# Performance work log

Measured on AMD Instinct MI355X. Metric: run time of the kernel, lower is better.

Reference implementation:

```python
import jax, jax.numpy as jnp
import numpy as np

B, T, D, H = 4, 2048, 1024, 16
HD = D // H  # head_size = 64


def setup_inputs() -> dict:
    key = jax.random.key(0)
    ks = jax.random.split(key, 6)
    s = 0.02
    x = jax.random.normal(ks[0], (B, T, D), dtype=jnp.float32)
    # per-head unfused projections, stacked over heads: [H, D, HD]
    Wq = jax.random.normal(ks[1], (H, D, HD), dtype=jnp.float32) * s
    Wk = jax.random.normal(ks[2], (H, D, HD), dtype=jnp.float32) * s
    Wv = jax.random.normal(ks[3], (H, D, HD), dtype=jnp.float32) * s
    # output projection, torch Linear layout [out, in]
    Wo = jax.random.normal(ks[4], (D, D), dtype=jnp.float32) * s
    bo = jax.random.normal(ks[5], (D,), dtype=jnp.float32) * s
    return {"x": x, "Wq": Wq, "Wk": Wk, "Wv": Wv, "Wo": Wo, "bo": bo}


def reference(x, Wq, Wk, Wv, Wo, bo):
    b, t, d = x.shape
    hd = Wq.shape[-1]
    q = jnp.einsum('btd,hdk->bhtk', x, Wq)
    k = jnp.einsum('btd,hdk->bhtk', x, Wk)
    v = jnp.einsum('btd,hdk->bhtk', x, Wv)
    scores = jnp.einsum('bhtk,bhsk->bhts', q, k) / jnp.sqrt(jnp.float32(hd))
    mask = jnp.tril(jnp.ones((t, t), dtype=bool))  # causal
    scores = jnp.where(mask, scores, jnp.float32(-jnp.inf))
    p = jax.nn.softmax(scores, axis=-1)
    o = jnp.einsum('bhts,bhsk->bhtk', p, v)
    o = o.transpose(0, 2, 1, 3).reshape(b, t, d)  # concat heads
    return o @ Wo.T + bo
```

## Files before the change

### kernel.cpp

```cpp
#include <hip/hip_runtime.h>
#include <hip/hip_bf16.h>
#include <stdint.h>

#define B_   4
#define T_   2048
#define D_   1024
#define H_   16
#define HD_  64
#define MROWS (B_*T_)
#define NQKV  3072
#define NST  (T_/64)

typedef __attribute__((ext_vector_type(8))) short  short8;
typedef __attribute__((ext_vector_type(4))) short  bf16x4;
typedef __attribute__((ext_vector_type(4))) float  floatx4;

#define QSCALE 0.1803368801111244f

__device__ inline void async_copy16(const __hip_bfloat16* g, __hip_bfloat16* l) {
  __builtin_amdgcn_global_load_lds(
      (const __attribute__((address_space(1))) void*)g,
      (__attribute__((address_space(3))) void*)l, 16, 0, 0);
}

__device__ inline floatx4 mfma16(bf16x4 a, bf16x4 b, floatx4 c) {
#if __has_builtin(__builtin_amdgcn_mfma_f32_16x16x16bf16_1k)
  return __builtin_amdgcn_mfma_f32_16x16x16bf16_1k(a, b, c, 0, 0, 0);
#elif __has_builtin(__builtin_amdgcn_mfma_f32_16x16x16_bf16)
  return __builtin_amdgcn_mfma_f32_16x16x16_bf16(a, b, c, 0, 0, 0);
#else
  short8 a8 = (short8){a[0], a[1], a[2], a[3], 0, 0, 0, 0};
  short8 b8 = (short8){b[0], b[1], b[2], b[3], 0, 0, 0, 0};
  return __builtin_amdgcn_mfma_f32_16x16x32_bf16(a8, b8, c, 0, 0, 0);
#endif
}

__global__ void prep(const float* __restrict__ x, const float* __restrict__ Wo,
                     const float* __restrict__ Wq, const float* __restrict__ Wk,
                     const float* __restrict__ Wv,
                     __hip_bfloat16* __restrict__ xb, __hip_bfloat16* __restrict__ wob,
                     __hip_bfloat16* __restrict__ wqkv) {
  __shared__ __hip_bfloat16 tile[64][65];
  const int bid = (int)blockIdx.x;
  const int t = threadIdx.x;
  if (bid < 8192) {
    int i = (bid * 256 + t) * 4;
    float4 v = *(const float4*)(x + i);
    xb[i + 0] = __float2bfloat16(v.x);
    xb[i + 1] = __float2bfloat16(v.y);
    xb[i + 2] = __float2bfloat16(v.z);
    xb[i + 3] = __float2bfloat16(v.w);
  } else if (bid < 9216) {
    int i = ((bid - 8192) * 256 + t) * 4;
    float4 v = *(const float4*)(Wo + i);
    wob[i + 0] = __float2bfloat16(v.x);
    wob[i + 1] = __float2bfloat16(v.y);
    wob[i + 2] = __float2bfloat16(v.z);
    wob[i + 3] = __float2bfloat16(v.w);
  } else {
    int idx = bid - 9216;
    const int d0 = (idx & 15) * 64;
    const int wh = idx >> 4;
    const int which = wh >> 4, h = wh & 15;
    const float* W = (which == 0) ? Wq : ((which == 1) ? Wk : Wv);
    const float* base = W + (size_t)h * D_ * HD_;
#pragma unroll
    for (int i = 0; i < 16; i++) {
      int e = i * 256 + t;
      int dr = e >> 6, hd = e & 63;
      tile[dr][hd] = __float2bfloat16(base[(size_t)(d0 + dr) * HD_ + hd]);
    }
    __syncthreads();
#pragma unroll
    for (int i = 0; i < 16; i++) {
      int e = i * 256 + t;
      int hd = e >> 6, dr = e & 63;
      wqkv[(size_t)(which * 1024 + h * 64 + hd) * D_ + d0 + dr] = tile[dr][hd];
    }
  }
}

__global__ void repack_kv(const __hip_bfloat16* __restrict__ qkv,
                          __hip_bfloat16* __restrict__ kpack, __hip_bfloat16* __restrict__ vpack) {
  __shared__ __hip_bfloat16 Ks[64][72];
  __shared__ __hip_bfloat16 Vs[64][72];
  const int tid = threadIdx.x;
  const int st = blockIdx.x, bh = blockIdx.y;
  const int b = bh >> 4, h = bh & 15;
#pragma unroll
  for (int p = 0; p < 2; p++) {
    int c = p * 256 + tid;
    int row = c >> 3, col8 = c & 7;
    const __hip_bfloat16* src = qkv + (size_t)(b * T_ + st * 64 + row) * NQKV + h * HD_ + col8 * 8;
    *(uint4*)&Ks[row][col8 * 8] = *(const uint4*)(src + 1024);
    *(uint4*)&Vs[row][col8 * 8] = *(const uint4*)(src + 2048);
  }
  __syncthreads();
  const size_t base = ((size_t)bh * NST + st) * 8 * 512;
#pragma unroll
  for (int p = 0; p < 2; p++) {
    int pair = p * 256 + tid;
    int c = pair >> 6, l = pair & 63;
    int lq = l & 15, q = l >> 4;
    int ni = c >> 1, half = c & 1;
    short8 v = *(const short8*)&Ks[ni * 16 + lq][half * 32 + q * 8];
    *(short8*)(kpack + base + (size_t)c * 512 + l * 8) = v;
  }
#pragma unroll
  for (int p = 0; p < 2; p++) {
    int pair = p * 256 + tid;
    int c = pair >> 6, l = pair & 63;
    int lq = l & 15, q = l >> 4;
    int m = c >> 2, nt = c & 3;
    __hip_bfloat16 tmp[8];
#pragma unroll
    for (int half = 0; half < 2; half++)
#pragma unroll
      for (int j = 0; j < 4; j++)
        tmp[half * 4 + j] = Vs[(2 * m + half) * 16 + q * 4 + j][nt * 16 + lq];
    *(short8*)(vpack + base + (size_t)c * 512 + l * 8) = *(short8*)tmp;
  }
}


__device__ inline void stage16k(const __hip_bfloat16* __restrict__ grow0, int K,
                                short* ldst, int tid) {
#pragma unroll
  for (int l = 0; l < 2; ++l) {
    int c = l * 512 + tid;
    int r = c >> 3;
    int sw = (c & 7) ^ (r & 7);
    async_copy16(grow0 + (size_t)r * K + sw * 8, (__hip_bfloat16*)(ldst + c * 8));
  }
}

__device__ inline short8 fragld2(const short* base, int r, int slot) {
  return *(const short8*)(base + r * 64 + (((slot) ^ (r & 7)) << 3));
}

__launch_bounds__(512, 2)
__global__ void gemmq(const __hip_bfloat16* __restrict__ A, const __hip_bfloat16* __restrict__ Bt,
                      __hip_bfloat16* __restrict__ Cb, int M, int N, int K, float qscale) {
  __shared__ short LDS[2][32768];
  const int tid = threadIdx.x;
  const int lane = tid & 63, wid = tid >> 6;
  const int lq = lane & 15, quad = lane >> 4;
  const int wr = wid >> 2, wc = wid & 3;

  const int lin = (int)blockIdx.x;
  const int s = (lin & 7) * 64 + (lin >> 3);
  const int m0 = (s & 63) * 128, n0 = (s >> 6) * 384;

  const int NT = K >> 6;

  floatx4 acc[4][6];
#pragma unroll
  for (int i = 0; i < 4; i++)
#pragma unroll
    for (int j = 0; j < 6; j++) acc[i][j] = (floatx4){0.f, 0.f, 0.f, 0.f};

  {
    short* b0 = &LDS[0][0];
    stage16k(A + (size_t)m0 * K, K, b0, tid);
#pragma unroll
    for (int j = 0; j < 3; ++j)
      stage16k(Bt + (size_t)(n0 + 128 * j) * K, K, b0 + 8192 + 8192 * j, tid);
  }

#pragma unroll 1
  for (int t = 0; t < NT; ++t) {
    __syncthreads();
    const short* buf = &LDS[t & 1][0];
    short* nb = &LDS[(t & 1) ^ 1][0];
    const int kc = (t + 1) << 6;

    short8 a0[4], b0[6];
#pragma unroll
    for (int mi = 0; mi < 4; ++mi)
      a0[mi] = fragld2(buf, wr * 64 + mi * 16 + lq, quad);
#pragma unroll
    for (int ni = 0; ni < 6; ++ni)
      b0[ni] = fragld2(buf + 8192, wc * 96 + ni * 16 + lq, quad);
    if (t + 1 < NT) {
      stage16k(A + (size_t)m0 * K + kc, K, nb, tid);
#pragma unroll
      for (int j = 0; j < 3; ++j)
        stage16k(Bt + (size_t)(n0 + 128 * j) * K + kc, K, nb + 8192 + 8192 * j, tid);
    }
    __builtin_amdgcn_s_setprio(1);
#pragma unroll
    for (int mi = 0; mi < 4; ++mi)
#pragma unroll
      for (int ni = 0; ni < 6; ++ni)
        acc[mi][ni] = __builtin_amdgcn_mfma_f32_16x16x32_bf16(a0[mi], b0[ni], acc[mi][ni], 0, 0, 0);
    __builtin_amdgcn_s_setprio(0);

    short8 a1[4], b1[6];
#pragma unroll
    for (int mi = 0; mi < 4; ++mi)
      a1[mi] = fragld2(buf, wr * 64 + mi * 16 + lq, 4 + quad);
#pragma unroll
    for (int ni = 0; ni < 6; ++ni)
      b1[ni] = fragld2(buf + 8192, wc * 96 + ni * 16 + lq, 4 + quad);
    __builtin_amdgcn_s_setprio(1);
#pragma unroll
    for (int mi = 0; mi < 4; ++mi)
#pragma unroll
      for (int ni = 0; ni < 6; ++ni)
        acc[mi][ni] = __builtin_amdgcn_mfma_f32_16x16x32_bf16(a1[mi], b1[ni], acc[mi][ni], 0, 0, 0);
    __builtin_amdgcn_s_setprio(0);
  }

#pragma unroll
  for (int mi = 0; mi < 4; ++mi) {
#pragma unroll
    for (int ni = 0; ni < 6; ++ni) {
      int col = n0 + wc * 96 + ni * 16 + lq;
      float sc = (col < 1024) ? qscale : 1.0f;
#pragma unroll
      for (int r = 0; r < 4; ++r) {
        int row = m0 + wr * 64 + mi * 16 + quad * 4 + r;
        Cb[(size_t)row * N + col] = __float2bfloat16(acc[mi][ni][r] * sc);
      }
    }
  }
}

__launch_bounds__(512, 2)
__global__ void gemmo(const __hip_bfloat16* __restrict__ A, const __hip_bfloat16* __restrict__ Bt,
                      float* __restrict__ Cf, const float* __restrict__ bias,
                      int M, int N, int K) {
  __shared__ short LDS[2][24576];
  const int tid = threadIdx.x;
  const int lane = tid & 63, wid = tid >> 6;
  const int lq = lane & 15, quad = lane >> 4;
  const int wr = wid >> 2, wc = wid & 3;

  const int lin = (int)blockIdx.x;
  const int s = (lin & 7) * 32 + (lin >> 3);
  const int m0 = (s & 63) * 128, n0 = (s >> 6) * 256;

  const int NT = K >> 6;

  floatx4 acc[4][4];
#pragma unroll
  for (int i = 0; i < 4; i++)
#pragma unroll
    for (int j = 0; j < 4; j++) acc[i][j] = (floatx4){0.f, 0.f, 0.f, 0.f};

  {
    short* b0 = &LDS[0][0];
    stage16k(A + (size_t)m0 * K, K, b0, tid);
    stage16k(Bt + (size_t)n0 * K, K, b0 + 8192, tid);
    stage16k(Bt + (size_t)(n0 + 128) * K, K, b0 + 16384, tid);
  }

#pragma unroll 1
  for (int t = 0; t < NT; ++t) {
    __syncthreads();
    const short* buf = &LDS[t & 1][0];
    short* nb = &LDS[(t & 1) ^ 1][0];
    const int kc = (t + 1) << 6;

    short8 a0[4], b0[4];
#pragma unroll
    for (int mi = 0; mi < 4; ++mi)
      a0[mi] = fragld2(buf, wr * 64 + mi * 16 + lq, quad);
#pragma unroll
    for (int ni = 0; ni < 4; ++ni)
      b0[ni] = fragld2(buf + 8192, wc * 64 + ni * 16 + lq, quad);
    if (t + 1 < NT) {
      stage16k(A + (size_t)m0 * K + kc, K, nb, tid);
      stage16k(Bt + (size_t)n0 * K + kc, K, nb + 8192, tid);
      stage16k(Bt + (size_t)(n0 + 128) * K + kc, K, nb + 16384, tid);
    }
    __builtin_amdgcn_s_setprio(1);
#pragma unroll
    for (int mi = 0; mi < 4; ++mi)
#pragma unroll
      for (int ni = 0; ni < 4; ++ni)
        acc[mi][ni] = __builtin_amdgcn_mfma_f32_16x16x32_bf16(a0[mi], b0[ni], acc[mi][ni], 0, 0, 0);
    __builtin_amdgcn_s_setprio(0);

    short8 a1[4], b1[4];
#pragma unroll
    for (int mi = 0; mi < 4; ++mi)
      a1[mi] = fragld2(buf, wr * 64 + mi * 16 + lq, 4 + quad);
#pragma unroll
    for (int ni = 0; ni < 4; ++ni)
      b1[ni] = fragld2(buf + 8192, wc * 64 + ni * 16 + lq, 4 + quad);
    __builtin_amdgcn_s_setprio(1);
#pragma unroll
    for (int mi = 0; mi < 4; ++mi)
#pragma unroll
      for (int ni = 0; ni < 4; ++ni)
        acc[mi][ni] = __builtin_amdgcn_mfma_f32_16x16x32_bf16(a1[mi], b1[ni], acc[mi][ni], 0, 0, 0);
    __builtin_amdgcn_s_setprio(0);
  }

#pragma unroll
  for (int mi = 0; mi < 4; ++mi) {
#pragma unroll
    for (int ni = 0; ni < 4; ++ni) {
      int col = n0 + wc * 64 + ni * 16 + lq;
      float bv = bias[col];
#pragma unroll
      for (int r = 0; r < 4; ++r) {
        int row = m0 + wr * 64 + mi * 16 + quad * 4 + r;
        Cf[(size_t)row * N + col] = acc[mi][ni][r] + bv;
      }
    }
  }
}

__launch_bounds__(256, 2)
__global__ void attn(const __hip_bfloat16* __restrict__ qkv,
                     const __hip_bfloat16* __restrict__ kpack,
                     const __hip_bfloat16* __restrict__ vpack,
                     __hip_bfloat16* __restrict__ obuf) {
  __shared__ __hip_bfloat16 KVs[2][8192];
  const int tid = threadIdx.x;
  const int w = tid >> 6, lane = tid & 63;
  const int lq = lane & 15, quad = lane >> 4;

  const int bh = (int)blockIdx.x;
  const int a  = (int)blockIdx.y;
  const int b = bh >> 4, h = bh & 15;

  const __hip_bfloat16* kbase = kpack + ((size_t)bh * NST) * 4096;
  const __hip_bfloat16* vbase = vpack + ((size_t)bh * NST) * 4096;

#pragma unroll 1
  for (int seg = 0; seg < 2; ++seg) {
    const int tbase = seg ? (NST - 2 - 2 * a) : (2 * a);
    const int qt = tbase + (w >> 1);
    const int rbase = (w & 1) * 32;

    short8 qf[2][2];
#pragma unroll
    for (int bi = 0; bi < 2; bi++) {
      const __hip_bfloat16* qp =
          qkv + ((size_t)(b * T_ + qt * 64 + rbase + bi * 16 + lq)) * NQKV + h * HD_;
      qf[bi][0] = *(const short8*)(qp + quad * 8);
      qf[bi][1] = *(const short8*)(qp + 32 + quad * 8);
    }

    floatx4 Oacc[2][4];
#pragma unroll
    for (int bi = 0; bi < 2; bi++)
#pragma unroll
      for (int i = 0; i < 4; i++) Oacc[bi][i] = (floatx4){0.f, 0.f, 0.f, 0.f};
    float lrow[2] = {0.f, 0.f};

    const int itTop = tbase + 1;

#pragma unroll
    for (int j = 0; j < 2; ++j) {
      int c = j * 256 + tid;
      async_copy16(kbase + (size_t)c * 8, &KVs[0][0] + c * 8);
      async_copy16(vbase + (size_t)c * 8, &KVs[0][4096] + c * 8);
    }
    __syncthreads();

#pragma unroll 1
    for (int it = 0; it <= itTop; ++it) {
      const int cur = it & 1;
      if (it < itTop) {
        const __hip_bfloat16* kn = kbase + (size_t)(it + 1) * 4096;
        const __hip_bfloat16* vn = vbase + (size_t)(it + 1) * 4096;
#pragma unroll
        for (int j = 0; j < 2; ++j) {
          int c = j * 256 + tid;
          async_copy16(kn + (size_t)c * 8, &KVs[cur ^ 1][0] + c * 8);
          async_copy16(vn + (size_t)c * 8, &KVs[cur ^ 1][4096] + c * 8);
        }
      }
      if (it <= qt) {
        const __hip_bfloat16* Kb = &KVs[cur][0] + lane * 8;
        const __hip_bfloat16* Vb = &KVs[cur][4096] + lane * 8;
        short8 kf[4], kg[4];
#pragma unroll
        for (int ni = 0; ni < 4; ni++) {
          kf[ni] = *(const short8*)(Kb + (size_t)(ni * 2 + 0) * 512);
          kg[ni] = *(const short8*)(Kb + (size_t)(ni * 2 + 1) * 512);
        }
        short8 vfr[8];
#pragma unroll
        for (int c = 0; c < 8; c++) vfr[c] = *(const short8*)(Vb + (size_t)c * 512);

        floatx4 Sc[2][4];
        __builtin_amdgcn_s_setprio(1);
#pragma unroll
        for (int bi = 0; bi < 2; bi++)
#pragma unroll
          for (int ni = 0; ni < 4; ni++) {
            floatx4 c0 = (floatx4){0.f, 0.f, 0.f, 0.f};
            c0 = __builtin_amdgcn_mfma_f32_16x16x32_bf16(kf[ni], qf[bi][0], c0, 0, 0, 0);
            c0 = __builtin_amdgcn_mfma_f32_16x16x32_bf16(kg[ni], qf[bi][1], c0, 0, 0, 0);
            Sc[bi][ni] = c0;
          }
        __builtin_amdgcn_s_setprio(0);

        if (it == qt) {
#pragma unroll
          for (int bi = 0; bi < 2; bi++) {
            int lrow_idx = rbase + bi * 16 + lq;
#pragma unroll
            for (int ni = 0; ni < 4; ni++)
#pragma unroll
              for (int r = 0; r < 4; r++) {
                int s_loc = ni * 16 + quad * 4 + r;
                if (s_loc > lrow_idx) Sc[bi][ni][r] = -__builtin_inff();
              }
          }
        }

        bf16x4 pf[2][4];
#pragma unroll
        for (int bi = 0; bi < 2; bi++)
#pragma unroll
          for (int c = 0; c < 4; c++) {
            __hip_bfloat16 pb[4];
#pragma unroll
            for (int r = 0; r < 4; r++) {
              float p = __builtin_amdgcn_exp2f(Sc[bi][c][r]);
              lrow[bi] += p;
              pb[r] = __float2bfloat16(p);
            }
            pf[bi][c] = *(bf16x4*)pb;
          }

        __builtin_amdgcn_s_setprio(1);
#pragma unroll
        for (int m = 0; m < 2; m++)
#pragma unroll
          for (int nt = 0; nt < 4; nt++) {
            short8 v8 = vfr[m * 4 + nt];
            bf16x4 vlo = (bf16x4){v8[0], v8[1], v8[2], v8[3]};
            bf16x4 vhi = (bf16x4){v8[4], v8[5], v8[6], v8[7]};
#pragma unroll
            for (int bi = 0; bi < 2; bi++) {
              Oacc[bi][nt] = mfma16(pf[bi][2 * m + 0], vlo, Oacc[bi][nt]);
              Oacc[bi][nt] = mfma16(pf[bi][2 * m + 1], vhi, Oacc[bi][nt]);
            }
          }
        __builtin_amdgcn_s_setprio(0);
      }
      __syncthreads();
    }

#pragma unroll
    for (int bi = 0; bi < 2; bi++) {
      float ps = lrow[bi];
      ps += __shfl_xor(ps, 16);
      ps += __shfl_xor(ps, 32);
      float inv = 1.0f / ps;
#pragma unroll
      for (int r = 0; r < 4; r++) {
        float invr = __shfl(inv, quad * 4 + r);
        int t = qt * 64 + rbase + bi * 16 + quad * 4 + r;
#pragma unroll
        for (int nt = 0; nt < 4; nt++)
          obuf[(size_t)(b * T_ + t) * D_ + h * HD_ + nt * 16 + lq] =
              __float2bfloat16(Oacc[bi][nt][r] * invr);
      }
    }
  }
}


extern "C" void kernel_launch(void* const* d_in, const int* in_sizes, int n_in,
                              void* d_out, int out_size, void* d_ws, size_t ws_size,
                              hipStream_t stream) {
  const float* x  = (const float*)d_in[0];
  const float* Wq = (const float*)d_in[1];
  const float* Wk = (const float*)d_in[2];
  const float* Wv = (const float*)d_in[3];
  const float* Wo = (const float*)d_in[4];
  const float* bo = (const float*)d_in[5];
  float* out = (float*)d_out;

  char* ws = (char*)d_ws;
  __hip_bfloat16* xb    = (__hip_bfloat16*)(ws);
  __hip_bfloat16* obuf  = (__hip_bfloat16*)(ws);
  __hip_bfloat16* wqkv  = (__hip_bfloat16*)(ws + ((size_t)16 << 20));
  __hip_bfloat16* wob   = (__hip_bfloat16*)(ws + ((size_t)22 << 20));
  __hip_bfloat16* qkv   = (__hip_bfloat16*)(ws + ((size_t)24 << 20));
  __hip_bfloat16* kpack = (__hip_bfloat16*)(ws + ((size_t)72 << 20));
  __hip_bfloat16* vpack = (__hip_bfloat16*)(ws + ((size_t)88 << 20));

  prep<<<9984, 256, 0, stream>>>(x, Wo, Wq, Wk, Wv, xb, wob, wqkv);

  gemmq<<<512, 512, 0, stream>>>(xb, wqkv, qkv, MROWS, NQKV, D_, QSCALE);

  repack_kv<<<dim3(NST, B_ * H_), 256, 0, stream>>>(qkv, kpack, vpack);

  attn<<<dim3(B_ * H_, 8), 256, 0, stream>>>(qkv, kpack, vpack, obuf);

  gemmo<<<256, 512, 0, stream>>>(obuf, wob, out, bo, MROWS, D_, D_);
}
```

Baseline: 247.9 us.

## Double KV tile per attention stage and retile output GEMM to 128x128

```diff
diff --git a/kernel.cpp b/kernel.cpp
--- a/kernel.cpp
+++ b/kernel.cpp
@@ -123,11 +123,12 @@
 }
 
 
+template <int THR>
 __device__ inline void stage16k(const __hip_bfloat16* __restrict__ grow0, int K,
                                 short* ldst, int tid) {
 #pragma unroll
-  for (int l = 0; l < 2; ++l) {
-    int c = l * 512 + tid;
+  for (int l = 0; l < 1024 / THR; ++l) {
+    int c = l * THR + tid;
     int r = c >> 3;
     int sw = (c & 7) ^ (r & 7);
     async_copy16(grow0 + (size_t)r * K + sw * 8, (__hip_bfloat16*)(ldst + c * 8));
@@ -161,10 +162,10 @@
 
   {
     short* b0 = &LDS[0][0];
-    stage16k(A + (size_t)m0 * K, K, b0, tid);
+    stage16k<512>(A + (size_t)m0 * K, K, b0, tid);
 #pragma unroll
     for (int j = 0; j < 3; ++j)
-      stage16k(Bt + (size_t)(n0 + 128 * j) * K, K, b0 + 8192 + 8192 * j, tid);
+      stage16k<512>(Bt + (size_t)(n0 + 128 * j) * K, K, b0 + 8192 + 8192 * j, tid);
   }
 
 #pragma unroll 1
@@ -182,10 +183,10 @@
     for (int ni = 0; ni < 6; ++ni)
       b0[ni] = fragld2(buf + 8192, wc * 96 + ni * 16 + lq, quad);
     if (t + 1 < NT) {
-      stage16k(A + (size_t)m0 * K + kc, K, nb, tid);
+      stage16k<512>(A + (size_t)m0 * K + kc, K, nb, tid);
 #pragma unroll
       for (int j = 0; j < 3; ++j)
-        stage16k(Bt + (size_t)(n0 + 128 * j) * K + kc, K, nb + 8192 + 8192 * j, tid);
+        stage16k<512>(Bt + (size_t)(n0 + 128 * j) * K + kc, K, nb + 8192 + 8192 * j, tid);
     }
     __builtin_amdgcn_s_setprio(1);
 #pragma unroll
@@ -226,19 +227,19 @@
   }
 }
 
-__launch_bounds__(512, 2)
-__global__ void gemmo(const __hip_bfloat16* __restrict__ A, const __hip_bfloat16* __restrict__ Bt,
+__launch_bounds__(256, 2)
+__global__ void gemmp(const __hip_bfloat16* __restrict__ A, const __hip_bfloat16* __restrict__ Bt,
                       float* __restrict__ Cf, const float* __restrict__ bias,
                       int M, int N, int K) {
-  __shared__ short LDS[2][24576];
+  __shared__ short LDS[2][16384];
   const int tid = threadIdx.x;
   const int lane = tid & 63, wid = tid >> 6;
   const int lq = lane & 15, quad = lane >> 4;
-  const int wr = wid >> 2, wc = wid & 3;
+  const int wr = wid >> 1, wc = wid & 1;
 
   const int lin = (int)blockIdx.x;
-  const int s = (lin & 7) * 32 + (lin >> 3);
-  const int m0 = (s & 63) * 128, n0 = (s >> 6) * 256;
+  const int s = (lin & 7) * 64 + (lin >> 3);
+  const int m0 = (s & 63) * 128, n0 = (s >> 6) * 128;
 
   const int NT = K >> 6;
 
@@ -248,12 +249,8 @@
 #pragma unroll
     for (int j = 0; j < 4; j++) acc[i][j] = (floatx4){0.f, 0.f, 0.f, 0.f};
 
-  {
-    short* b0 = &LDS[0][0];
-    stage16k(A + (size_t)m0 * K, K, b0, tid);
-    stage16k(Bt + (size_t)n0 * K, K, b0 + 8192, tid);
-    stage16k(Bt + (size_t)(n0 + 128) * K, K, b0 + 16384, tid);
-  }
+  stage16k<256>(A + (size_t)m0 * K, K, &LDS[0][0], tid);
+  stage16k<256>(Bt + (size_t)n0 * K, K, &LDS[0][8192], tid);
 
 #pragma unroll 1
   for (int t = 0; t < NT; ++t) {
@@ -270,9 +267,8 @@
     for (int ni = 0; ni < 4; ++ni)
       b0[ni] = fragld2(buf + 8192, wc * 64 + ni * 16 + lq, quad);
     if (t + 1 < NT) {
-      stage16k(A + (size_t)m0 * K + kc, K, nb, tid);
-      stage16k(Bt + (size_t)n0 * K + kc, K, nb + 8192, tid);
-      stage16k(Bt + (size_t)(n0 + 128) * K + kc, K, nb + 16384, tid);
+      stage16k<256>(A + (size_t)m0 * K + kc, K, nb, tid);
+      stage16k<256>(Bt + (size_t)n0 * K + kc, K, nb + 8192, tid);
     }
     __builtin_amdgcn_s_setprio(1);
 #pragma unroll
@@ -318,7 +314,7 @@
                      const __hip_bfloat16* __restrict__ kpack,
                      const __hip_bfloat16* __restrict__ vpack,
                      __hip_bfloat16* __restrict__ obuf) {
-  __shared__ __hip_bfloat16 KVs[2][8192];
+  __shared__ __hip_bfloat16 KVs[2][16384];
   const int tid = threadIdx.x;
   const int w = tid >> 6, lane = tid & 63;
   const int lq = lane & 15, quad = lane >> 4;
@@ -352,101 +348,108 @@
       for (int i = 0; i < 4; i++) Oacc[bi][i] = (floatx4){0.f, 0.f, 0.f, 0.f};
     float lrow[2] = {0.f, 0.f};
 
-    const int itTop = tbase + 1;
-
-#pragma unroll
-    for (int j = 0; j < 2; ++j) {
+    const int pTop = tbase >> 1;
+
+#pragma unroll
+    for (int j = 0; j < 4; ++j) {
       int c = j * 256 + tid;
       async_copy16(kbase + (size_t)c * 8, &KVs[0][0] + c * 8);
-      async_copy16(vbase + (size_t)c * 8, &KVs[0][4096] + c * 8);
-    }
-    __syncthreads();
-
+      async_copy16(vbase + (size_t)c * 8, &KVs[0][8192] + c * 8);
+    }
+    asm volatile("s_waitcnt vmcnt(0)" ::: "memory");
+    __builtin_amdgcn_s_barrier();
+
+    int cur = 0;
 #pragma unroll 1
-    for (int it = 0; it <= itTop; ++it) {
-      const int cur = it & 1;
-      if (it < itTop) {
-        const __hip_bfloat16* kn = kbase + (size_t)(it + 1) * 4096;
-        const __hip_bfloat16* vn = vbase + (size_t)(it + 1) * 4096;
-#pragma unroll
-        for (int j = 0; j < 2; ++j) {
+    for (int p = 0; p <= pTop; ++p) {
+      if (p < pTop) {
+        const __hip_bfloat16* kn = kbase + (size_t)(2 * (p + 1)) * 4096;
+        const __hip_bfloat16* vn = vbase + (size_t)(2 * (p + 1)) * 4096;
+#pragma unroll
+        for (int j = 0; j < 4; ++j) {
           int c = j * 256 + tid;
           async_copy16(kn + (size_t)c * 8, &KVs[cur ^ 1][0] + c * 8);
-          async_copy16(vn + (size_t)c * 8, &KVs[cur ^ 1][4096] + c * 8);
+          async_copy16(vn + (size_t)c * 8, &KVs[cur ^ 1][8192] + c * 8);
         }
       }
-      if (it <= qt) {
-        const __hip_bfloat16* Kb = &KVs[cur][0] + lane * 8;
-        const __hip_bfloat16* Vb = &KVs[cur][4096] + lane * 8;
-        short8 kf[4], kg[4];
-#pragma unroll
-        for (int ni = 0; ni < 4; ni++) {
-          kf[ni] = *(const short8*)(Kb + (size_t)(ni * 2 + 0) * 512);
-          kg[ni] = *(const short8*)(Kb + (size_t)(ni * 2 + 1) * 512);
-        }
-        short8 vfr[8];
-#pragma unroll
-        for (int c = 0; c < 8; c++) vfr[c] = *(const short8*)(Vb + (size_t)c * 512);
-
-        floatx4 Sc[2][4];
-        __builtin_amdgcn_s_setprio(1);
-#pragma unroll
-        for (int bi = 0; bi < 2; bi++)
+#pragma unroll
+      for (int f = 0; f < 2; ++f) {
+        const int t64 = 2 * p + f;
+        if (t64 <= qt) {
+          const __hip_bfloat16* Kb = &KVs[cur][f * 4096] + lane * 8;
+          const __hip_bfloat16* Vb = &KVs[cur][8192 + f * 4096] + lane * 8;
+          short8 kf[4], kg[4];
 #pragma unroll
           for (int ni = 0; ni < 4; ni++) {
-            floatx4 c0 = (floatx4){0.f, 0.f, 0.f, 0.f};
-            c0 = __builtin_amdgcn_mfma_f32_16x16x32_bf16(kf[ni], qf[bi][0], c0, 0, 0, 0);
-            c0 = __builtin_amdgcn_mfma_f32_16x16x32_bf16(kg[ni], qf[bi][1], c0, 0, 0, 0);
-            Sc[bi][ni] = c0;
+            kf[ni] = *(const short8*)(Kb + (size_t)(ni * 2 + 0) * 512);
+            kg[ni] = *(const short8*)(Kb + (size_t)(ni * 2 + 1) * 512);
           }
-        __builtin_amdgcn_s_setprio(0);
-
-        if (it == qt) {
-#pragma unroll
-          for (int bi = 0; bi < 2; bi++) {
-            int lrow_idx = rbase + bi * 16 + lq;
-#pragma unroll
-            for (int ni = 0; ni < 4; ni++)
-#pragma unroll
-              for (int r = 0; r < 4; r++) {
-                int s_loc = ni * 16 + quad * 4 + r;
-                if (s_loc > lrow_idx) Sc[bi][ni][r] = -__builtin_inff();
-              }
-          }
-        }
-
-        bf16x4 pf[2][4];
-#pragma unroll
-        for (int bi = 0; bi < 2; bi++)
-#pragma unroll
-          for (int c = 0; c < 4; c++) {
-            __hip_bfloat16 pb[4];
-#pragma unroll
-            for (int r = 0; r < 4; r++) {
-              float p = __builtin_amdgcn_exp2f(Sc[bi][c][r]);
-              lrow[bi] += p;
-              pb[r] = __float2bfloat16(p);
+          short8 vfr[8];
+#pragma unroll
+          for (int c = 0; c < 8; c++) vfr[c] = *(const short8*)(Vb + (size_t)c * 512);
+
+          floatx4 Sc[2][4];
+          __builtin_amdgcn_s_setprio(1);
+#pragma unroll
+          for (int bi = 0; bi < 2; bi++)
+#pragma unroll
+            for (int ni = 0; ni < 4; ni++) {
+              floatx4 c0 = (floatx4){0.f, 0.f, 0.f, 0.f};
+              c0 = __builtin_amdgcn_mfma_f32_16x16x32_bf16(kf[ni], qf[bi][0], c0, 0, 0, 0);
+              c0 = __builtin_amdgcn_mfma_f32_16x16x32_bf16(kg[ni], qf[bi][1], c0, 0, 0, 0);
+              Sc[bi][ni] = c0;
             }
-            pf[bi][c] = *(bf16x4*)pb;
-          }
-
-        __builtin_amdgcn_s_setprio(1);
-#pragma unroll
-        for (int m = 0; m < 2; m++)
-#pragma unroll
-          for (int nt = 0; nt < 4; nt++) {
-            short8 v8 = vfr[m * 4 + nt];
-            bf16x4 vlo = (bf16x4){v8[0], v8[1], v8[2], v8[3]};
-            bf16x4 vhi = (bf16x4){v8[4], v8[5], v8[6], v8[7]};
+          __builtin_amdgcn_s_setprio(0);
+
+          if (t64 == qt) {
 #pragma unroll
             for (int bi = 0; bi < 2; bi++) {
-              Oacc[bi][nt] = mfma16(pf[bi][2 * m + 0], vlo, Oacc[bi][nt]);
-              Oacc[bi][nt] = mfma16(pf[bi][2 * m + 1], vhi, Oacc[bi][nt]);
+              int lrow_idx = rbase + bi * 16 + lq;
+#pragma unroll
+              for (int ni = 0; ni < 4; ni++)
+#pragma unroll
+                for (int r = 0; r < 4; r++) {
+                  int s_loc = ni * 16 + quad * 4 + r;
+                  if (s_loc > lrow_idx) Sc[bi][ni][r] = -__builtin_inff();
+                }
             }
           }
-        __builtin_amdgcn_s_setprio(0);
+
+          bf16x4 pf[2][4];
+#pragma unroll
+          for (int bi = 0; bi < 2; bi++)
+#pragma unroll
+            for (int c = 0; c < 4; c++) {
+              __hip_bfloat16 pb[4];
+#pragma unroll
+              for (int r = 0; r < 4; r++) {
+                float pv = __builtin_amdgcn_exp2f(Sc[bi][c][r]);
+                lrow[bi] += pv;
+                pb[r] = __float2bfloat16(pv);
+              }
+              pf[bi][c] = *(bf16x4*)pb;
+            }
+
+          __builtin_amdgcn_s_setprio(1);
+#pragma unroll
+          for (int m = 0; m < 2; m++)
+#pragma unroll
+            for (int nt = 0; nt < 4; nt++) {
+              short8 v8 = vfr[m * 4 + nt];
+              bf16x4 vlo = (bf16x4){v8[0], v8[1], v8[2], v8[3]};
+              bf16x4 vhi = (bf16x4){v8[4], v8[5], v8[6], v8[7]};
+#pragma unroll
+              for (int bi = 0; bi < 2; bi++) {
+                Oacc[bi][nt] = mfma16(pf[bi][2 * m + 0], vlo, Oacc[bi][nt]);
+                Oacc[bi][nt] = mfma16(pf[bi][2 * m + 1], vhi, Oacc[bi][nt]);
+              }
+            }
+          __builtin_amdgcn_s_setprio(0);
+        }
       }
-      __syncthreads();
+      if (p < pTop) { asm volatile("s_waitcnt vmcnt(0)" ::: "memory"); }
+      __builtin_amdgcn_s_barrier();
+      cur ^= 1;
     }
 
 #pragma unroll
@@ -497,5 +500,5 @@
 
   attn<<<dim3(B_ * H_, 8), 256, 0, stream>>>(qkv, kpack, vpack, obuf);
 
-  gemmo<<<256, 512, 0, stream>>>(obuf, wob, out, bo, MROWS, D_, D_);
-}
+  gemmp<<<512, 256, 0, stream>>>(obuf, wob, out, bo, MROWS, D_, D_);
+}
```

After: 238.9 us. -3.6%, faster.
